# Performance work log

Measured on AMD Instinct MI355X. Metric: run time of the kernel, lower is better.

Reference implementation:

```python
import jax, jax.numpy as jnp
import numpy as np

B, S, I, H, M, V = 32, 128, 512, 512, 256, 100000


def setup_inputs() -> dict:
    key = jax.random.key(0)
    k0, k1, k2, k3 = jax.random.split(key, 4)
    return {
        "x": jax.random.normal(k0, (B, S, I), dtype=jnp.float32),
        "token_ids": jax.random.randint(k1, (B, S), 0, V, dtype=jnp.int32),
        "W_ih": jax.random.normal(k2, (4 * H, I), dtype=jnp.float32) * 0.05,
        "W_hh": jax.random.normal(k3, (4 * H, H), dtype=jnp.float32) * 0.05,
        "b_ih": jnp.zeros((4 * H,), jnp.float32),
        "b_hh": jnp.zeros((4 * H,), jnp.float32),
        "mem_table": jnp.zeros((V, M), jnp.float32),  # word_memory_forward, zeros = initial_memory
    }


def reference(x, token_ids, W_ih, W_hh, b_ih, b_hh, mem_table):
    # x: [B, S, I] (batch_first), token_ids: [B, S] keys into external memory.
    hid = W_hh.shape[1]
    msz = mem_table.shape[1]
    base = hid - msz  # previous_cell_size in the original

    def word_step(carry, inp):
        h, c, mem = carry          # h,c: [H], mem: [V, M]
        xt, tok = inp              # xt: [I], tok: scalar int
        # splice per-token memory into the cell state (read)
        c = jnp.concatenate([c[:base], mem[tok]])
        # torch LSTMCell: gates = x W_ih^T + b_ih + h W_hh^T + b_hh, order i,f,g,o
        gates = xt @ W_ih.T + b_ih + h @ W_hh.T + b_hh
        i, f, g, o = jnp.split(gates, 4)
        i = jax.nn.sigmoid(i); f = jax.nn.sigmoid(f)
        g = jnp.tanh(g); o = jax.nn.sigmoid(o)
        c2 = f * c + i * g
        h2 = o * jnp.tanh(c2)
        # write updated memory slice back (scatter)
        mem = mem.at[tok].set(c2[base:])
        return (h2, c2, mem), h2

    def sentence_step(mem, sent):
        xs, toks = sent            # xs: [S, I], toks: [S]
        h0 = jnp.zeros((hid,), x.dtype)
        c0 = jnp.zeros((hid,), x.dtype)
        (h_last, c_last, mem2), hs = jax.lax.scan(word_step, (h0, c0, mem), (xs, toks))
        return mem2, (hs, h_last)

    # sentences processed sequentially, sharing one external memory table
    _, (hs, last) = jax.lax.scan(sentence_step, mem_table, (x, token_ids))
    return hs, last  # [B, S, H], [B, H]
```

## Files before the change

### kernel.cpp

```cpp
#include <hip/hip_runtime.h>
#include <hip/hip_bf16.h>


#define T_TOTAL 4096
#define Ssz 128
#define HID 512
#define RDIM 2048
#define KDIM 512
#define MSZ 256
#define NX (1 << 21)

typedef unsigned long long u64;
typedef unsigned int u32;
typedef unsigned short u16;
typedef _Float16 f16;
typedef __attribute__((ext_vector_type(8))) _Float16 f16x8;
typedef __attribute__((ext_vector_type(4))) float f32x4;

__device__ __forceinline__ u16 f2h(float x) {
  union { f16 h; u16 u; } c; c.h = (f16)x; return c.u;
}
__device__ __forceinline__ float h2f(u16 b) {
  union { f16 h; u16 u; } c; c.u = b; return (float)c.h;
}
__device__ __forceinline__ float sigm_f(float x) {
  return __builtin_amdgcn_rcpf(1.f + __expf(-x));
}
__device__ __forceinline__ float tanh_f(float x) {
  return 1.f - 2.f * __builtin_amdgcn_rcpf(1.f + __expf(2.f * x));
}

__device__ __forceinline__ u32 ld32_dev(const u32* p) {
  u32 v;
  asm volatile("global_load_dword %0, %1, off sc0 sc1\n\ts_waitcnt vmcnt(0)"
               : "=v"(v) : "v"(p) : "memory");
  return v;
}
__device__ __forceinline__ void st32_dev(u32* p, u32 v) {
  asm volatile("global_store_dword %0, %1, off sc0 sc1" :: "v"(p), "v"(v) : "memory");
}
__device__ __forceinline__ u64 ld64_dev(const u64* p) {
  u64 v;
  asm volatile("global_load_dwordx2 %0, %1, off sc0 sc1\n\ts_waitcnt vmcnt(0)"
               : "=v"(v) : "v"(p) : "memory");
  return v;
}
__device__ __forceinline__ void st64_dev(u64* p, u64 v) {
  asm volatile("global_store_dwordx2 %0, %1, off sc0 sc1" :: "v"(p), "v"(v) : "memory");
}

__global__ __launch_bounds__(256) void cvt_f16(
    const float* __restrict__ X, const float* __restrict__ W,
    u16* __restrict__ dst)
{
  const int i = (blockIdx.x * 256 + threadIdx.x) * 4;
  const float* s = (i < NX) ? &X[i] : &W[i - NX];
  const float4 v = *(const float4*)s;
  ushort4 o;
  o.x = f2h(v.x); o.y = f2h(v.y); o.z = f2h(v.z); o.w = f2h(v.w);
  *(ushort4*)&dst[i] = o;
}

__global__ __launch_bounds__(256) void gemm_mfma(
    const u16* __restrict__ Xh, const u16* __restrict__ Wh,
    const float* __restrict__ b_ih, const float* __restrict__ b_hh,
    u16* __restrict__ Gb)
{
  const int tid = threadIdx.x;
  const int wave = tid >> 6;
  const int lane = tid & 63;
  const int wm = wave >> 1, wn = wave & 1;
  const int m0 = blockIdx.x * 64 + wm * 32;
  const int n0 = blockIdx.y * 64 + wn * 32;
  const int fr = lane & 15;
  const int kc = lane >> 4;

  f32x4 acc[2][2] = {};
  const u16* ax0 = &Xh[(size_t)(m0 + fr) * KDIM + kc * 8];
  const u16* ax1 = ax0 + 16 * KDIM;
  const u16* bx0 = &Wh[(size_t)(n0 + fr) * KDIM + kc * 8];
  const u16* bx1 = bx0 + 16 * KDIM;
#pragma unroll
  for (int k0 = 0; k0 < KDIM; k0 += 32) {
    const f16x8 a0 = *(const f16x8*)(ax0 + k0);
    const f16x8 a1 = *(const f16x8*)(ax1 + k0);
    const f16x8 b0 = *(const f16x8*)(bx0 + k0);
    const f16x8 b1 = *(const f16x8*)(bx1 + k0);
    acc[0][0] = __builtin_amdgcn_mfma_f32_16x16x32_f16(a0, b0, acc[0][0], 0, 0, 0);
    acc[0][1] = __builtin_amdgcn_mfma_f32_16x16x32_f16(a0, b1, acc[0][1], 0, 0, 0);
    acc[1][0] = __builtin_amdgcn_mfma_f32_16x16x32_f16(a1, b0, acc[1][0], 0, 0, 0);
    acc[1][1] = __builtin_amdgcn_mfma_f32_16x16x32_f16(a1, b1, acc[1][1], 0, 0, 0);
  }
#pragma unroll
  for (int jn = 0; jn < 2; ++jn) {
    const int col = n0 + jn * 16 + fr;
    const float bb = b_ih[col] + b_hh[col];
#pragma unroll
    for (int i = 0; i < 2; ++i) {
#pragma unroll
      for (int rr = 0; rr < 4; ++rr) {
        const int row = m0 + i * 16 + kc * 4 + rr;
        Gb[(size_t)row * RDIM + col] = f2h(acc[i][jn][rr] + bb);
      }
    }
  }
}

__global__ __launch_bounds__(256) void prep_prev(
    const int* __restrict__ tok, int* __restrict__ prev)
{
  __shared__ int tl[T_TOTAL];
  for (int i = threadIdx.x; i < T_TOTAL; i += 256) tl[i] = tok[i];
  __syncthreads();
  const int t = blockIdx.x * 256 + threadIdx.x;
  const int my = tl[t];
  int p = -1;
  for (int u = t - 1; u >= 0; --u)
    if (tl[u] == my) { p = u; break; }
  prev[t] = p;
}

__global__ __launch_bounds__(512, 2) void lstm_pipe(
    const u16* __restrict__ Gb, const float* __restrict__ Whh,
    const int* __restrict__ prev,
    u64* __restrict__ mbox,
    u32* __restrict__ hslot,
    float* __restrict__ hs, float* __restrict__ last)
{
  const int bid = blockIdx.x;
  const int g  = bid & 31;
  const int wl = bid >> 5;
  const int tid = threadIdx.x;
  const int wv = tid >> 6;
  const int ln = tid & 63;
  const int fr = ln & 15;
  const int kb = ln >> 4;

  __shared__ u16 hh[HID];
  __shared__ float gsum[256];

  f16x8 areg[2][16];
#pragma unroll
  for (int b = 0; b < 2; ++b) {
    const int rb = wv * 2 + b;
    const int gg2 = rb >> 2, jb = rb & 3;
    const int grow = gg2 * HID + wl * 64 + jb * 16 + fr;
#pragma unroll
    for (int kc = 0; kc < 16; ++kc) {
      const float* src = &Whh[(size_t)grow * KDIM + kc * 32 + kb * 8];
      const float4 f0 = *(const float4*)src;
      const float4 f1 = *(const float4*)(src + 4);
      f16x8 a;
      a[0] = (f16)f0.x; a[1] = (f16)f0.y; a[2] = (f16)f0.z; a[3] = (f16)f0.w;
      a[4] = (f16)f1.x; a[5] = (f16)f1.y; a[6] = (f16)f1.z; a[7] = (f16)f1.w;
      areg[b][kc] = a;
    }
  }

  const int pc = (wv <= wl) ? wv - 1 : wv;

  u32* hsl = hslot + ((size_t)g << 10);
  const int j = wl * 64 + tid;
  const int mcol = (wl - 4) * 64 + tid;

  float c_reg = 0.f;

  for (int s = 0; s < Ssz; ++s) {
    const int t = g * Ssz + s;

    u16 g0 = 0, g1 = 0, g2 = 0, g3 = 0;
    int pt = -1; u64 mv = 0;
    if (tid < 64) {
      const u16* gr = &Gb[(size_t)t * RDIM + wl * 64 + tid];
      g0 = gr[0]; g1 = gr[512]; g2 = gr[1024]; g3 = gr[1536];
      if (wl >= 4) {
        pt = prev[t];
        if (pt >= 0) mv = ld64_dev(&mbox[(size_t)pt * MSZ + mcol]);
      }
    }

    if (s == 0) {
      hh[tid] = 0;
    } else if (wv >= 1) {
      u32* sp = &hsl[((s & 1) << 9) + pc * 64 + ln];
      u32 v = ld32_dev(sp);
      while (!__all((v >> 16) == (u32)s)) {
        __builtin_amdgcn_s_sleep(1);
        v = ld32_dev(sp);
      }
      hh[pc * 64 + ln] = (u16)v;
    }
    __syncthreads();

    f32x4 acc0a = {}, acc0b = {}, acc1a = {}, acc1b = {};
    f16x8 bv = {};
#pragma unroll
    for (int kc = 0; kc < 8; ++kc) {
      if (fr == 0) bv = *(const f16x8*)&hh[kc * 32 + kb * 8];
      acc0a = __builtin_amdgcn_mfma_f32_16x16x32_f16(areg[0][kc], bv, acc0a, 0, 0, 0);
      acc1a = __builtin_amdgcn_mfma_f32_16x16x32_f16(areg[1][kc], bv, acc1a, 0, 0, 0);
    }
#pragma unroll
    for (int kc = 8; kc < 16; ++kc) {
      if (fr == 0) bv = *(const f16x8*)&hh[kc * 32 + kb * 8];
      acc0b = __builtin_amdgcn_mfma_f32_16x16x32_f16(areg[0][kc], bv, acc0b, 0, 0, 0);
      acc1b = __builtin_amdgcn_mfma_f32_16x16x32_f16(areg[1][kc], bv, acc1b, 0, 0, 0);
    }
    if (fr == 0) {
      const f32x4 acc0 = acc0a + acc0b;
      const f32x4 acc1 = acc1a + acc1b;
      *(f32x4*)&gsum[(wv * 2 + 0) * 16 + kb * 4] = acc0;
      *(f32x4*)&gsum[(wv * 2 + 1) * 16 + kb * 4] = acc1;
    }
    __syncthreads();

    if (tid < 64) {
      const float zi = gsum[tid]       + h2f(g0);
      const float zf = gsum[64 + tid]  + h2f(g1);
      const float zg = gsum[128 + tid] + h2f(g2);
      const float zo = gsum[192 + tid] + h2f(g3);
      const float i_ = sigm_f(zi);
      const float f_ = sigm_f(zf);
      const float g_ = tanh_f(zg);
      const float o_ = sigm_f(zo);
      float cv;
      if (wl >= 4) {
        if (pt >= 0) {
          while ((u32)(mv >> 32) != 1u) {
            __builtin_amdgcn_s_sleep(2);
            mv = ld64_dev(&mbox[(size_t)pt * MSZ + mcol]);
          }
          cv = __uint_as_float((u32)mv);
        } else {
          cv = 0.f;
        }
      } else {
        cv = (s == 0) ? 0.f : c_reg;
      }
      const float c2 = f_ * cv + i_ * g_;
      const float h2 = o_ * tanh_f(c2);
      c_reg = c2;

      st32_dev(&hsl[(((s + 1) & 1) << 9) + j], ((u32)(s + 1) << 16) | (u32)f2h(h2));
      if (wl >= 4)
        st64_dev(&mbox[(size_t)t * MSZ + mcol],
                 (1ull << 32) | (u64)__float_as_uint(c2));
      hh[j] = f2h(h2);
      hs[(size_t)t * HID + j] = h2;
      if (s == Ssz - 1) last[(size_t)g * HID + j] = h2;
    }
  }
}

extern "C" void kernel_launch(void* const* d_in, const int* in_sizes, int n_in,
                              void* d_out, int out_size, void* d_ws, size_t ws_size,
                              hipStream_t stream) {
  const float* x     = (const float*)d_in[0];
  const int*   tok   = (const int*)d_in[1];
  const float* W_ih  = (const float*)d_in[2];
  const float* W_hh  = (const float*)d_in[3];
  const float* b_ih  = (const float*)d_in[4];
  const float* b_hh  = (const float*)d_in[5];
  float*       out   = (float*)d_out;

  char* ws = (char*)d_ws;
  u64* mbox   = (u64*)ws;
  u32* hslot  = (u32*)(ws + 8388608);
  int* prev   = (int*)(ws + 8519680);
  u16* XW     = (u16*)(ws + 8536064);
  u16* Xh     = XW;
  u16* Wh     = XW + NX;
  u16* Gb     = (u16*)(ws + 14827520);


  cvt_f16<<<3072, 256, 0, stream>>>(x, W_ih, XW);
  prep_prev<<<T_TOTAL / 256, 256, 0, stream>>>(tok, prev);
  gemm_mfma<<<dim3(T_TOTAL / 64, RDIM / 64), 256, 0, stream>>>(Xh, Wh, b_ih, b_hh, Gb);
  lstm_pipe<<<256, 512, 0, stream>>>(Gb, W_hh, prev, mbox, hslot,
                                     out, out + (size_t)T_TOTAL * HID);
}
```

Measured before the change: 963.4 us.

## Compute LSTM cell update in MFMA lanes, removing gsum barrier and double-buffering h

Each wave's W_hh row mapping is reordered so the i/f/g/o gates for the same hidden units end up in its own MFMA accumulators, paired via lane shuffles. The cell update is then computed directly by a few lanes per wave, with vectorized stores of h, memory and outputs. This removes the shared gsum buffer and the second __syncthreads per timestep. The h buffer is double-buffered to avoid a write-after-read race, and prep_prev becomes a branchless forward scan.

```diff
diff --git a/kernel.cpp b/kernel.cpp
--- a/kernel.cpp
+++ b/kernel.cpp
@@ -16,6 +16,7 @@
 typedef _Float16 f16;
 typedef __attribute__((ext_vector_type(8))) _Float16 f16x8;
 typedef __attribute__((ext_vector_type(4))) float f32x4;
+typedef __attribute__((ext_vector_type(4))) u32 u32x4;
 
 __device__ __forceinline__ u16 f2h(float x) {
   union { f16 h; u16 u; } c; c.h = (f16)x; return c.u;
@@ -36,17 +37,29 @@
                : "=v"(v) : "v"(p) : "memory");
   return v;
 }
-__device__ __forceinline__ void st32_dev(u32* p, u32 v) {
-  asm volatile("global_store_dword %0, %1, off sc0 sc1" :: "v"(p), "v"(v) : "memory");
-}
-__device__ __forceinline__ u64 ld64_dev(const u64* p) {
-  u64 v;
-  asm volatile("global_load_dwordx2 %0, %1, off sc0 sc1\n\ts_waitcnt vmcnt(0)"
-               : "=v"(v) : "v"(p) : "memory");
-  return v;
-}
-__device__ __forceinline__ void st64_dev(u64* p, u64 v) {
-  asm volatile("global_store_dwordx2 %0, %1, off sc0 sc1" :: "v"(p), "v"(v) : "memory");
+__device__ __forceinline__ void ld_c4(const u64* p, u64 m[4]) {
+  u32x4 a, b;
+  asm volatile("global_load_dwordx4 %0, %2, off sc0 sc1\n\t"
+               "global_load_dwordx4 %1, %2, off offset:16 sc0 sc1\n\t"
+               "s_waitcnt vmcnt(0)"
+               : "=&v"(a), "=&v"(b) : "v"(p) : "memory");
+  m[0] = ((u64)a[1] << 32) | a[0];
+  m[1] = ((u64)a[3] << 32) | a[2];
+  m[2] = ((u64)b[1] << 32) | b[0];
+  m[3] = ((u64)b[3] << 32) | b[2];
+}
+__device__ __forceinline__ void st_c4(u64* p, const u64 m[4]) {
+  u32x4 a, b;
+  a[0] = (u32)m[0]; a[1] = (u32)(m[0] >> 32);
+  a[2] = (u32)m[1]; a[3] = (u32)(m[1] >> 32);
+  b[0] = (u32)m[2]; b[1] = (u32)(m[2] >> 32);
+  b[2] = (u32)m[3]; b[3] = (u32)(m[3] >> 32);
+  asm volatile("global_store_dwordx4 %0, %1, off sc0 sc1\n\t"
+               "global_store_dwordx4 %0, %2, off offset:16 sc0 sc1"
+               :: "v"(p), "v"(a), "v"(b) : "memory");
+}
+__device__ __forceinline__ void st_h4(u32* p, u32x4 v) {
+  asm volatile("global_store_dwordx4 %0, %1, off sc0 sc1" :: "v"(p), "v"(v) : "memory");
 }
 
 __global__ __launch_bounds__(256) void cvt_f16(
@@ -115,8 +128,9 @@
   const int t = blockIdx.x * 256 + threadIdx.x;
   const int my = tl[t];
   int p = -1;
-  for (int u = t - 1; u >= 0; --u)
-    if (tl[u] == my) { p = u; break; }
+#pragma unroll 8
+  for (int u = 0; u < t; ++u)
+    p = (tl[u] == my) ? u : p;
   prev[t] = p;
 }
 
@@ -136,15 +150,12 @@
   const int fr = ln & 15;
   const int kb = ln >> 4;
 
-  __shared__ u16 hh[HID];
-  __shared__ float gsum[256];
+  __shared__ u16 hh[2][HID];
 
   f16x8 areg[2][16];
 #pragma unroll
   for (int b = 0; b < 2; ++b) {
-    const int rb = wv * 2 + b;
-    const int gg2 = rb >> 2, jb = rb & 3;
-    const int grow = gg2 * HID + wl * 64 + jb * 16 + fr;
+    const int grow = (2 * b + (fr >> 3)) * HID + wl * 64 + wv * 8 + (fr & 7);
 #pragma unroll
     for (int kc = 0; kc < 16; ++kc) {
       const float* src = &Whh[(size_t)grow * KDIM + kc * 32 + kb * 8];
@@ -158,29 +169,30 @@
   }
 
   const int pc = (wv <= wl) ? wv - 1 : wv;
-
   u32* hsl = hslot + ((size_t)g << 10);
-  const int j = wl * 64 + tid;
-  const int mcol = (wl - 4) * 64 + tid;
-
-  float c_reg = 0.f;
+
+  const bool cellln = (fr == 0) && (kb < 2);
+  const int jb = (ln & 16) ? 4 : 0;
+  const int gsel = (ln >> 5) & 1;
+  const int jcol = wl * 64 + wv * 8 + jb;
+  const int mc = (wl - 4) * 64 + wv * 8 + jb;
+
+  f32x4 c_reg;
+  c_reg[0] = 0.f; c_reg[1] = 0.f; c_reg[2] = 0.f; c_reg[3] = 0.f;
 
   for (int s = 0; s < Ssz; ++s) {
     const int t = g * Ssz + s;
 
-    u16 g0 = 0, g1 = 0, g2 = 0, g3 = 0;
-    int pt = -1; u64 mv = 0;
-    if (tid < 64) {
-      const u16* gr = &Gb[(size_t)t * RDIM + wl * 64 + tid];
-      g0 = gr[0]; g1 = gr[512]; g2 = gr[1024]; g3 = gr[1536];
-      if (wl >= 4) {
-        pt = prev[t];
-        if (pt >= 0) mv = ld64_dev(&mbox[(size_t)pt * MSZ + mcol]);
-      }
+    const ushort4 G0 = *(const ushort4*)&Gb[(size_t)t * RDIM + gsel * HID + jcol];
+    const ushort4 G1 = *(const ushort4*)&Gb[(size_t)t * RDIM + (2 + gsel) * HID + jcol];
+    int pt = -1; u64 m4[4] = {0, 0, 0, 0};
+    if (wl >= 4 && cellln) {
+      pt = prev[t];
+      if (pt >= 0) ld_c4(&mbox[(size_t)pt * MSZ + mc], m4);
     }
 
     if (s == 0) {
-      hh[tid] = 0;
+      hh[0][tid] = 0;
     } else if (wv >= 1) {
       u32* sp = &hsl[((s & 1) << 9) + pc * 64 + ln];
       u32 v = ld32_dev(sp);
@@ -188,66 +200,78 @@
         __builtin_amdgcn_s_sleep(1);
         v = ld32_dev(sp);
       }
-      hh[pc * 64 + ln] = (u16)v;
+      hh[s & 1][pc * 64 + ln] = (u16)v;
     }
     __syncthreads();
 
-    f32x4 acc0a = {}, acc0b = {}, acc1a = {}, acc1b = {};
+    f32x4 a0a = {}, a0b = {}, a1a = {}, a1b = {};
     f16x8 bv = {};
+    const u16* hbuf = hh[s & 1];
 #pragma unroll
     for (int kc = 0; kc < 8; ++kc) {
-      if (fr == 0) bv = *(const f16x8*)&hh[kc * 32 + kb * 8];
-      acc0a = __builtin_amdgcn_mfma_f32_16x16x32_f16(areg[0][kc], bv, acc0a, 0, 0, 0);
-      acc1a = __builtin_amdgcn_mfma_f32_16x16x32_f16(areg[1][kc], bv, acc1a, 0, 0, 0);
+      if (fr == 0) bv = *(const f16x8*)&hbuf[kc * 32 + kb * 8];
+      a0a = __builtin_amdgcn_mfma_f32_16x16x32_f16(areg[0][kc], bv, a0a, 0, 0, 0);
+      a1a = __builtin_amdgcn_mfma_f32_16x16x32_f16(areg[1][kc], bv, a1a, 0, 0, 0);
     }
 #pragma unroll
     for (int kc = 8; kc < 16; ++kc) {
-      if (fr == 0) bv = *(const f16x8*)&hh[kc * 32 + kb * 8];
-      acc0b = __builtin_amdgcn_mfma_f32_16x16x32_f16(areg[0][kc], bv, acc0b, 0, 0, 0);
-      acc1b = __builtin_amdgcn_mfma_f32_16x16x32_f16(areg[1][kc], bv, acc1b, 0, 0, 0);
-    }
-    if (fr == 0) {
-      const f32x4 acc0 = acc0a + acc0b;
-      const f32x4 acc1 = acc1a + acc1b;
-      *(f32x4*)&gsum[(wv * 2 + 0) * 16 + kb * 4] = acc0;
-      *(f32x4*)&gsum[(wv * 2 + 1) * 16 + kb * 4] = acc1;
-    }
-    __syncthreads();
-
-    if (tid < 64) {
-      const float zi = gsum[tid]       + h2f(g0);
-      const float zf = gsum[64 + tid]  + h2f(g1);
-      const float zg = gsum[128 + tid] + h2f(g2);
-      const float zo = gsum[192 + tid] + h2f(g3);
-      const float i_ = sigm_f(zi);
-      const float f_ = sigm_f(zf);
-      const float g_ = tanh_f(zg);
-      const float o_ = sigm_f(zo);
-      float cv;
+      if (fr == 0) bv = *(const f16x8*)&hbuf[kc * 32 + kb * 8];
+      a0b = __builtin_amdgcn_mfma_f32_16x16x32_f16(areg[0][kc], bv, a0b, 0, 0, 0);
+      a1b = __builtin_amdgcn_mfma_f32_16x16x32_f16(areg[1][kc], bv, a1b, 0, 0, 0);
+    }
+    const f32x4 acc0 = a0a + a0b;
+    const f32x4 acc1 = a1a + a1b;
+
+    float z0[4], z1[4], zf[4], zo[4];
+#pragma unroll
+    for (int r = 0; r < 4; ++r) {
+      z0[r] = acc0[r] + h2f((&G0.x)[r]);
+      z1[r] = acc1[r] + h2f((&G1.x)[r]);
+    }
+#pragma unroll
+    for (int r = 0; r < 4; ++r) {
+      zf[r] = __shfl_xor(z0[r], 32, 64);
+      zo[r] = __shfl_xor(z1[r], 32, 64);
+    }
+
+    if (cellln) {
+      f32x4 cv;
       if (wl >= 4) {
         if (pt >= 0) {
-          while ((u32)(mv >> 32) != 1u) {
+          while (!((u32)(m4[0] >> 32) == 1u && (u32)(m4[1] >> 32) == 1u &&
+                   (u32)(m4[2] >> 32) == 1u && (u32)(m4[3] >> 32) == 1u)) {
             __builtin_amdgcn_s_sleep(2);
-            mv = ld64_dev(&mbox[(size_t)pt * MSZ + mcol]);
+            ld_c4(&mbox[(size_t)pt * MSZ + mc], m4);
           }
-          cv = __uint_as_float((u32)mv);
+          cv[0] = __uint_as_float((u32)m4[0]); cv[1] = __uint_as_float((u32)m4[1]);
+          cv[2] = __uint_as_float((u32)m4[2]); cv[3] = __uint_as_float((u32)m4[3]);
         } else {
-          cv = 0.f;
+          cv[0] = 0.f; cv[1] = 0.f; cv[2] = 0.f; cv[3] = 0.f;
         }
       } else {
-        cv = (s == 0) ? 0.f : c_reg;
+        cv = c_reg;
       }
-      const float c2 = f_ * cv + i_ * g_;
-      const float h2 = o_ * tanh_f(c2);
-      c_reg = c2;
-
-      st32_dev(&hsl[(((s + 1) & 1) << 9) + j], ((u32)(s + 1) << 16) | (u32)f2h(h2));
-      if (wl >= 4)
-        st64_dev(&mbox[(size_t)t * MSZ + mcol],
-                 (1ull << 32) | (u64)__float_as_uint(c2));
-      hh[j] = f2h(h2);
-      hs[(size_t)t * HID + j] = h2;
-      if (s == Ssz - 1) last[(size_t)g * HID + j] = h2;
+      u32x4 hp; u64 mo[4]; float4 hsv; ushort4 ho;
+#pragma unroll
+      for (int r = 0; r < 4; ++r) {
+        const float i_ = sigm_f(z0[r]);
+        const float f_ = sigm_f(zf[r]);
+        const float g_ = tanh_f(z1[r]);
+        const float o_ = sigm_f(zo[r]);
+        const float c2 = f_ * cv[r] + i_ * g_;
+        const float h2 = o_ * tanh_f(c2);
+        c_reg[r] = c2;
+        const u16 hb = f2h(h2);
+        hp[r] = ((u32)(s + 1) << 16) | (u32)hb;
+        mo[r] = (1ull << 32) | (u64)__float_as_uint(c2);
+        (&hsv.x)[r] = h2;
+        (&ho.x)[r] = hb;
+      }
+      st_h4(&hsl[(((s + 1) & 1) << 9) + jcol], hp);
+      if (wl >= 4) st_c4(&mbox[(size_t)t * MSZ + mc], mo);
+      *(ushort4*)&hh[(s + 1) & 1][jcol] = ho;
+      *(float4*)&hs[(size_t)t * HID + jcol] = hsv;
+      if (s == Ssz - 1) *(float4*)&last[(size_t)g * HID + jcol] = hsv;
     }
   }
 }
```

Result: faster. 880.1 us (-8.6%).
